# Performance work log

Hardware: AMD Instinct MI355X
Metric: run time of the kernel (lower is better)

## Reference

```python
import jax, jax.numpy as jnp
import numpy as np

EMBED = 768
HEADS = 12
HEAD_DIM = EMBED // HEADS
STREAMS = 4
SK_ITERS = 20
MLP_HIDDEN = 3072
EPS_SK = 1e-8
EPS_LN = 1e-5


def setup_inputs() -> dict:
    key = jax.random.key(0)
    ks = jax.random.split(key, 16)
    w = lambda k, shape: (jax.random.normal(k, shape, dtype=jnp.float32) * 0.02)
    return {
        "x": jax.random.normal(ks[0], (8, 1024, EMBED), dtype=jnp.float32),
        "ln1_g": jnp.ones((EMBED,), jnp.float32),
        "ln1_b": jnp.zeros((EMBED,), jnp.float32),
        "ln2_g": jnp.ones((EMBED,), jnp.float32),
        "ln2_b": jnp.zeros((EMBED,), jnp.float32),
        "qkv_w": w(ks[1], (3 * EMBED, EMBED)),
        "qkv_b": jnp.zeros((3 * EMBED,), jnp.float32),
        "proj_w": w(ks[2], (EMBED, EMBED)),
        "proj_b": jnp.zeros((EMBED,), jnp.float32),
        "fc1_w": w(ks[3], (MLP_HIDDEN, EMBED)),
        "fc1_b": jnp.zeros((MLP_HIDDEN,), jnp.float32),
        "fc2_w": w(ks[4], (EMBED, MLP_HIDDEN)),
        "fc2_b": jnp.zeros((EMBED,), jnp.float32),
        "a_hres": w(ks[5], (STREAMS, STREAMS)),
        "a_hpre": w(ks[6], (STREAMS,)),
        "a_hpost": w(ks[7], (STREAMS,)),
        "m_hres": w(ks[8], (STREAMS, STREAMS)),
        "m_hpre": w(ks[9], (STREAMS,)),
        "m_hpost": w(ks[10], (STREAMS,)),
    }


def layernorm(x, g, b):
    mu = x.mean(-1, keepdims=True)
    var = ((x - mu) ** 2).mean(-1, keepdims=True)
    return (x - mu) * jax.lax.rsqrt(var + EPS_LN) * g + b


def sinkhorn_knopp(logits):
    # logits: (n, n) -> doubly-stochastic (n, n); batch expansion in torch is redundant
    A = jnp.exp(logits)
    for _ in range(SK_ITERS):
        A = A / (A.sum(-1, keepdims=True) + EPS_SK)
        A = A / (A.sum(-2, keepdims=True) + EPS_SK)
    return A


def attention(x, qkv_w, qkv_b, proj_w, proj_b):
    B, N, D = x.shape
    qkv = x @ qkv_w.T + qkv_b                      # (B, N, 3D)
    qkv = qkv.reshape(B, N, 3, HEADS, HEAD_DIM)
    q, k, v = jnp.moveaxis(qkv, 2, 0)              # each (B, N, H, hd)
    scale = HEAD_DIM ** -0.5
    scores = jnp.einsum('bqhd,bkhd->bhqk', q, k) * scale
    attn = jax.nn.softmax(scores, axis=-1)
    out = jnp.einsum('bhqk,bkhd->bqhd', attn, v).reshape(B, N, D)
    return out @ proj_w.T + proj_b


def mlp(x, fc1_w, fc1_b, fc2_w, fc2_b):
    h = jax.nn.gelu(x @ fc1_w.T + fc1_b, approximate=False)
    return h @ fc2_w.T + fc2_b


def mhc(x, hres_logits, hpre_logits, hpost_logits, transform_fn):
    B, L, D = x.shape
    n, c = STREAMS, D // STREAMS
    xs = x.reshape(B, L, n, c)
    H_res = sinkhorn_knopp(hres_logits)            # (n, n)
    H_pre = jax.nn.softmax(hpre_logits)            # (n,)
    H_post = jax.nn.softmax(hpost_logits)          # (n,)
    x_pre = jnp.einsum('n,blnc->blc', H_pre, xs)   # weighted sum over streams
    x_pre_full = jnp.tile(x_pre, (1, 1, n))        # (B, L, D)
    t = transform_fn(x_pre_full)
    t_mean = t.reshape(B, L, n, c).mean(axis=2)    # (B, L, c)
    out = (jnp.einsum('nm,blmc->blnc', H_res, xs)
           + H_post[None, None, :, None] * t_mean[:, :, None, :])
    return out.reshape(B, L, D)


def reference(x, ln1_g, ln1_b, ln2_g, ln2_b, qkv_w, qkv_b, proj_w, proj_b,
              fc1_w, fc1_b, fc2_w, fc2_b,
              a_hres, a_hpre, a_hpost, m_hres, m_hpre, m_hpost):
    x = mhc(x, a_hres, a_hpre, a_hpost,
            lambda h: attention(layernorm(h, ln1_g, ln1_b), qkv_w, qkv_b, proj_w, proj_b))
    x = mhc(x, m_hres, m_hpre, m_hpost,
            lambda h: mlp(layernorm(h, ln2_g, ln2_b), fc1_w, fc1_b, fc2_w, fc2_b))
    return x
```

## Files before the change

kernel.cpp:

```cpp
#include <hip/hip_runtime.h>
#include <hip/hip_bf16.h>
#include <cstdint>
#include <cstddef>

#define EMBED 768
#define STREAMS 4
#define CHUNK 192
#define HEADS 12
#define HD 64
#define SEQ 1024
#define BATCH 8
#define TOKENS (BATCH * SEQ)
#define MLPH 3072

typedef __bf16 bf16;
typedef __bf16 bf16x4 __attribute__((ext_vector_type(4)));
typedef __bf16 bf16x8 __attribute__((ext_vector_type(8)));
typedef float f32x4 __attribute__((ext_vector_type(4)));
typedef float f32x16 __attribute__((ext_vector_type(16)));

#define GLDS16(gp, lp)                                                        \
  __builtin_amdgcn_global_load_lds(                                           \
      (const __attribute__((address_space(1))) void*)(gp),                    \
      (__attribute__((address_space(3))) void*)(lp), 16, 0, 0)

#define BARRIER() do { asm volatile("" ::: "memory");                         \
  __builtin_amdgcn_s_barrier(); asm volatile("" ::: "memory"); } while (0)

#define CVT_NQ 442368
#define CVT_NP 147456
#define CVT_N1 589824
#define CVT_TOT (CVT_NQ + CVT_NP + 2 * CVT_N1)
__global__ __launch_bounds__(256) void head_kernel(
    const float* __restrict__ x, const float* __restrict__ ln1_g,
    const float* __restrict__ ln1_b, bf16* __restrict__ LN,
    const float* __restrict__ qw, const float* __restrict__ pw,
    const float* __restrict__ f1w, const float* __restrict__ f2w,
    bf16* __restrict__ Wq, bf16* __restrict__ Wp,
    bf16* __restrict__ W1, bf16* __restrict__ W2,
    const float* ar, const float* ap, const float* ao,
    const float* mr, const float* mp, const float* mo, float* HS) {
  const int tid = threadIdx.x;
  if (blockIdx.x < 2048) {
    int i = blockIdx.x * 256 + tid;
    const int st = 2048 * 256;
    for (; i < CVT_TOT; i += st) {
      const float* src; bf16* dst; int off;
      if (i < CVT_NQ)                      { src = qw;  dst = Wq; off = i; }
      else if (i < CVT_NQ + CVT_NP)        { src = pw;  dst = Wp; off = i - CVT_NQ; }
      else if (i < CVT_NQ + CVT_NP + CVT_N1){ src = f1w; dst = W1; off = i - CVT_NQ - CVT_NP; }
      else                                 { src = f2w; dst = W2; off = i - CVT_NQ - CVT_NP - CVT_N1; }
      const float4 v = ((const float4*)src)[off];
      bf16x4 o = {(bf16)v.x, (bf16)v.y, (bf16)v.z, (bf16)v.w};
      *(bf16x4*)(dst + (size_t)off * 4) = o;
    }
    return;
  }
  if (blockIdx.x == 4096) {
    if (tid != 0) return;
    const float* L[2] = {ar, mr};
    const float* P[2] = {ap, mp};
    const float* O[2] = {ao, mo};
    for (int s = 0; s < 2; ++s) {
      float A[16];
      for (int i = 0; i < 16; ++i) A[i] = expf(L[s][i]);
      for (int it = 0; it < 20; ++it) {
        for (int r = 0; r < 4; ++r) {
          float rs = A[4*r] + A[4*r+1] + A[4*r+2] + A[4*r+3] + 1e-8f;
          for (int c = 0; c < 4; ++c) A[4*r+c] /= rs;
        }
        for (int c = 0; c < 4; ++c) {
          float cs = A[c] + A[4+c] + A[8+c] + A[12+c] + 1e-8f;
          for (int r = 0; r < 4; ++r) A[4*r+c] /= cs;
        }
      }
      float* dst = HS + s * 24;
      for (int i = 0; i < 16; ++i) dst[i] = A[i];
      {
        float m = fmaxf(fmaxf(P[s][0], P[s][1]), fmaxf(P[s][2], P[s][3]));
        float e[4], t = 0.f;
        for (int i = 0; i < 4; ++i) { e[i] = expf(P[s][i] - m); t += e[i]; }
        for (int i = 0; i < 4; ++i) dst[16 + i] = e[i] / t;
      }
      {
        float m = fmaxf(fmaxf(O[s][0], O[s][1]), fmaxf(O[s][2], O[s][3]));
        float e[4], t = 0.f;
        for (int i = 0; i < 4; ++i) { e[i] = expf(O[s][i] - m); t += e[i]; }
        for (int i = 0; i < 4; ++i) dst[20 + i] = e[i] / t;
      }
    }
    return;
  }
  const int t = (blockIdx.x - 2048) * 4 + (tid >> 6);
  const int l = tid & 63;
  float H0, H1, H2, H3;
  {
    const float p0 = ap[0], p1 = ap[1], p2 = ap[2], p3 = ap[3];
    const float m = fmaxf(fmaxf(p0, p1), fmaxf(p2, p3));
    const float e0 = __expf(p0 - m), e1 = __expf(p1 - m),
                e2 = __expf(p2 - m), e3 = __expf(p3 - m);
    const float inv = 1.f / (e0 + e1 + e2 + e3);
    H0 = e0 * inv; H1 = e1 * inv; H2 = e2 * inv; H3 = e3 * inv;
  }
  const float* xr = x + (size_t)t * EMBED;
  float sv[3];
  #pragma unroll
  for (int k = 0; k < 3; ++k) {
    const int c = l + 64 * k;
    sv[k] = H0*xr[c] + H1*xr[CHUNK+c] + H2*xr[2*CHUNK+c] + H3*xr[3*CHUNK+c];
  }
  float sum = sv[0] + sv[1] + sv[2];
  float sq  = sv[0]*sv[0] + sv[1]*sv[1] + sv[2]*sv[2];
  #pragma unroll
  for (int m = 1; m < 64; m <<= 1) {
    sum += __shfl_xor(sum, m);
    sq  += __shfl_xor(sq, m);
  }
  const float mu = sum * (1.f / CHUNK);
  const float rs = rsqrtf(sq * (1.f / CHUNK) - mu * mu + 1e-5f);
  bf16* orow = LN + (size_t)t * EMBED;
  #pragma unroll
  for (int k = 0; k < 3; ++k) {
    const int c = l + 64 * k;
    const float sn = (sv[k] - mu) * rs;
    #pragma unroll
    for (int n = 0; n < 4; ++n) {
      const int d = n * CHUNK + c;
      orow[d] = (bf16)(sn * ln1_g[d] + ln1_b[d]);
    }
  }
}

template <int GELU, int KSPLIT>
__global__ __launch_bounds__(256, 2) void gemm_bt(
    const bf16* __restrict__ A, const bf16* __restrict__ B,
    const float* __restrict__ bias, bf16* __restrict__ C0,
    bf16* __restrict__ C1, int M, int N, int K) {
  constexpr int BM = 128, BN = 128, BK = 32;
  __shared__ bf16 sA[3][BM * BK];
  __shared__ bf16 sB[3][BN * BK];
  const int tid  = threadIdx.x;
  const int lane = tid & 63;
  const int Lw = blockIdx.y * gridDim.x + blockIdx.x;
  const int bandRows = gridDim.y >> 3;
  const int j = Lw >> 3;
  const int colIdx = j / bandRows;
  const int rowLoc = j - colIdx * bandRows;
  const int bm = ((Lw & 7) * bandRows + rowLoc) * BM;
  const int bn = colIdx * BN;
  const int wave = tid >> 6;
  const int wr = (wave >> 1) * 64;
  const int wc = (wave & 1) * 64;
  f32x16 acc[2][2] = {};
  const int tr = tid >> 2;
  const int gt = tid & 3;
  const int gsw = (gt ^ ((tr >> 1) & 3)) * 8;
  const int kbeg = (KSPLIT > 1) ? blockIdx.z * (K / KSPLIT) : 0;
  const bf16* Ag = A + (size_t)(bm + tr) * K + kbeg + gsw;
  const bf16* Bg = B + (size_t)(bn + tr) * K + kbeg + gsw;
  const int lofs = tr * BK + gt * 8;
  const int r31 = lane & 31, rh = lane >> 5;
  const int asw = (r31 >> 1) & 3;
  const int nst = K / KSPLIT / BK;
#define STAGE(buf, t)                                                         \
  do { const int bk_ = (t) * BK;                                              \
    GLDS16(Ag + bk_, sA[buf] + lofs);                                         \
    GLDS16(Ag + (size_t)64 * K + bk_, sA[buf] + lofs + 64 * BK);              \
    GLDS16(Bg + bk_, sB[buf] + lofs);                                         \
    GLDS16(Bg + (size_t)64 * K + bk_, sB[buf] + lofs + 64 * BK);              \
  } while (0)
  STAGE(0, 0);
  STAGE(1, 1);
  int cur = 0;
  for (int t = 0; t < nst; ++t) {
    if (t + 2 < nst) {
      const int nb = cur + 2 >= 3 ? cur - 1 : cur + 2;
      STAGE(nb, t + 2);
      asm volatile("s_waitcnt vmcnt(8)" ::: "memory");
    } else if (t + 1 < nst) {
      asm volatile("s_waitcnt vmcnt(4)" ::: "memory");
    } else {
      asm volatile("s_waitcnt vmcnt(0)" ::: "memory");
    }
    BARRIER();
    bf16x8 af[2][2], bfr[2][2];
    #pragma unroll
    for (int ks = 0; ks < 2; ++ks) {
      const int pos = ((ks * 2 + rh) ^ asw) * 8;
      #pragma unroll
      for (int i = 0; i < 2; ++i) {
        af[i][ks]  = *(const bf16x8*)(sA[cur] + (wr + i * 32 + r31) * BK + pos);
        bfr[i][ks] = *(const bf16x8*)(sB[cur] + (wc + i * 32 + r31) * BK + pos);
      }
    }
    #pragma unroll
    for (int ks = 0; ks < 2; ++ks)
      #pragma unroll
      for (int i = 0; i < 2; ++i)
        #pragma unroll
        for (int j2 = 0; j2 < 2; ++j2)
          acc[i][j2] = __builtin_amdgcn_mfma_f32_32x32x16_bf16(af[i][ks], bfr[j2][ks], acc[i][j2], 0, 0, 0);
    BARRIER();
    cur = cur == 2 ? 0 : cur + 1;
  }
#undef STAGE
  const bool second = (KSPLIT > 1) && (blockIdx.z != 0);
  bf16* Co = second ? C1 : C0;
  #pragma unroll
  for (int j2 = 0; j2 < 2; ++j2) {
    const int col = bn + wc + j2 * 32 + r31;
    const float bv = second ? 0.f : bias[col];
    #pragma unroll
    for (int i = 0; i < 2; ++i) {
      const int row0 = bm + wr + i * 32 + 4 * rh;
      #pragma unroll
      for (int reg = 0; reg < 16; ++reg) {
        const int row = row0 + (reg & 3) + 8 * (reg >> 2);
        float v = acc[i][j2][reg] + bv;
        if (GELU) {
          float u = 0.7978845608f * (v + 0.044715f * v * v * v);
          u = fmaxf(fminf(u, 15.f), -15.f);
          const float e = __expf(-2.f * u);
          v = v / (1.f + e);
        }
        Co[(size_t)row * N + col] = (bf16)v;
      }
    }
  }
}

__global__ __launch_bounds__(256) void vt_kernel(const bf16* __restrict__ qkv,
                                                 bf16* __restrict__ VT) {
  const int tt = blockIdx.x;
  const int bh = blockIdx.y;
  const int bb = bh / HEADS;
  const int h = bh - bb * HEADS;
  __shared__ bf16 sT[64 * 64];
  const int t = threadIdx.x;
  const int srow = t >> 3;
  const int g = t & 7;
  const int gs = ((g ^ (srow & 7)) * 8);
  const bf16* Vg = qkv + ((size_t)(bb * SEQ + tt * 64 + srow)) * 2304 + 1536 + h * 64;
  GLDS16(Vg + gs, sT + srow * 64 + g * 8);
  GLDS16(Vg + (size_t)32 * 2304 + gs, sT + (32 + srow) * 64 + g * 8);
  __syncthreads();
  const int hd = t >> 2;
  const int tg = (t & 3) * 16;
  bf16 tmp[16];
  #pragma unroll
  for (int j = 0; j < 16; ++j) {
    const int tok = tg + j;
    tmp[j] = sT[tok * 64 + (hd ^ ((tok & 7) << 3))];
  }
  bf16* op = VT + (size_t)bh * (HD * SEQ) + (size_t)hd * SEQ + tt * 64 + tg;
  *(bf16x8*)(op) = *(const bf16x8*)(tmp);
  *(bf16x8*)(op + 8) = *(const bf16x8*)(tmp + 8);
}

__global__ __launch_bounds__(512) void attn_kernel(
    const bf16* __restrict__ qkv, const bf16* __restrict__ VT,
    bf16* __restrict__ out) {
  const int lin = blockIdx.x;
  const int qt = (lin >> 3) & 7;
  const int bh = (lin & 7) + 8 * (lin >> 6);
  const int bb = bh / HEADS;
  const int h = bh - bb * HEADS;
  const int tid = threadIdx.x;
  const int lane = tid & 63;
  const int wave = tid >> 6;
  const size_t tokBase = (size_t)bb * SEQ;
  const int q0 = qt * 128;

  __shared__ bf16 sQ[128 * 64];
  __shared__ bf16 sK[2][64 * 64];
  __shared__ bf16 sV[2][80 * 64];

  for (int idx = tid; idx < 16 * 64; idx += 512) {
    const bf16 v = (idx < 64) ? (bf16)1.f : (bf16)0.f;
    sV[0][64 * 64 + idx] = v;
    sV[1][64 * 64 + idx] = v;
  }

  {
    #pragma unroll
    for (int kq = 0; kq < 2; ++kq) {
      const int slot = tid + kq * 512;
      const int qr = slot >> 3;
      const int qg = slot & 7;
      const bf16* Qg = qkv + (tokBase + q0 + qr) * 2304 + h * 64;
      GLDS16(Qg + ((qg ^ (qr & 7)) * 8), sQ + qr * 64 + qg * 8);
    }
  }
  const int srow = tid >> 3;
  const int g = tid & 7;
  const int gs = ((g ^ (srow & 7)) * 8);
  const bf16* Kbase = qkv + tokBase * 2304 + 768 + h * 64;
  const bf16* Vbase = VT + (size_t)bh * (HD * SEQ);
  GLDS16(Kbase + (size_t)srow * 2304 + gs, sK[0] + srow * 64 + g * 8);
  GLDS16(Vbase + (size_t)srow * SEQ + gs, sV[0] + srow * 64 + g * 8);
  __syncthreads();

  const int l15 = lane & 15, hi = lane >> 4;
  const int ksw = (l15 & 7) << 3;
  bf16x8 qf[2];
  {
    const int qrow = wave * 16 + l15;
    const int qsw = (qrow & 7) << 3;
    #pragma unroll
    for (int ks = 0; ks < 2; ++ks)
      qf[ks] = *(const bf16x8*)(sQ + qrow * 64 + ((hi * 8 + ks * 32) ^ qsw));
  }
  asm volatile("s_waitcnt lgkmcnt(0)" ::: "memory");

  f32x4 o[5] = {};

  for (int it = 0; it < SEQ / 64; ++it) {
    const int cur = it & 1;
    if (it + 1 < SEQ / 64) {
      const int kb = (it + 1) * 64;
      GLDS16(Kbase + (size_t)(kb + srow) * 2304 + gs, sK[cur ^ 1] + srow * 64 + g * 8);
      GLDS16(Vbase + (size_t)srow * SEQ + kb + gs, sV[cur ^ 1] + srow * 64 + g * 8);
      asm volatile("s_waitcnt vmcnt(2)" ::: "memory");
    } else {
      asm volatile("s_waitcnt vmcnt(0)" ::: "memory");
    }
    BARRIER();
    f32x4 s[4];
    __builtin_amdgcn_s_setprio(1);
    #pragma unroll
    for (int nj = 0; nj < 4; ++nj) {
      s[nj] = (f32x4){0.f, 0.f, 0.f, 0.f};
      #pragma unroll
      for (int ks = 0; ks < 2; ++ks) {
        bf16x8 kf = *(const bf16x8*)(sK[cur] + (nj * 16 + l15) * 64 + ((hi * 8 + ks * 32) ^ ksw));
        s[nj] = __builtin_amdgcn_mfma_f32_16x16x32_bf16(qf[ks], kf, s[nj], 0, 0, 0);
      }
    }
    __builtin_amdgcn_s_setprio(0);
    bf16* Pw = sQ + wave * (16 * 64);
    #pragma unroll
    for (int r = 0; r < 4; ++r) {
      const int prow = hi * 4 + r;
      const int psw = (prow & 7) << 3;
      #pragma unroll
      for (int nj = 0; nj < 4; ++nj)
        Pw[prow * 64 + ((nj * 16 + l15) ^ psw)] = (bf16)__expf(s[nj][r] * 0.125f);
    }
    __builtin_amdgcn_s_setprio(1);
    #pragma unroll
    for (int ks = 0; ks < 2; ++ks) {
      bf16x8 pa = *(const bf16x8*)(Pw + l15 * 64 + ((hi * 8 + ks * 32) ^ ksw));
      #pragma unroll
      for (int nj = 0; nj < 5; ++nj) {
        bf16x8 vb = *(const bf16x8*)(sV[cur] + (nj * 16 + l15) * 64 + ((hi * 8 + ks * 32) ^ ksw));
        o[nj] = __builtin_amdgcn_mfma_f32_16x16x32_bf16(pa, vb, o[nj], 0, 0, 0);
      }
    }
    __builtin_amdgcn_s_setprio(0);
    BARRIER();
  }
  #pragma unroll
  for (int r = 0; r < 4; ++r) {
    const float lsum = __shfl(o[4][r], hi << 4, 64);
    const float inv = 1.f / lsum;
    const size_t row = tokBase + q0 + wave * 16 + hi * 4 + r;
    bf16* orow = out + row * EMBED + h * 64;
    #pragma unroll
    for (int nj = 0; nj < 4; ++nj)
      orow[nj * 16 + l15] = (bf16)(o[nj][r] * inv);
  }
}

template <int TWO>
__global__ __launch_bounds__(256) void combine_preln_kernel(
    const float* __restrict__ x, const bf16* __restrict__ t,
    const bf16* __restrict__ t2,
    const float* __restrict__ Hres, const float* __restrict__ Hpost,
    const float* __restrict__ Hpre2,
    const float* __restrict__ g2, const float* __restrict__ b2,
    bf16* __restrict__ X2, bf16* __restrict__ LN) {
  const int tok = blockIdx.x * 4 + (threadIdx.x >> 6);
  const int l = threadIdx.x & 63;
  const float* xr = x + (size_t)tok * EMBED;
  const bf16* tr = t + (size_t)tok * EMBED;
  const bf16* t2r = t2 + (size_t)tok * EMBED;
  bf16* orow = X2 + (size_t)tok * EMBED;
  const float Hr0 = Hres[0], Hr1 = Hres[1], Hr2 = Hres[2], Hr3 = Hres[3];
  const float Hr4 = Hres[4], Hr5 = Hres[5], Hr6 = Hres[6], Hr7 = Hres[7];
  const float Hr8 = Hres[8], Hr9 = Hres[9], HrA = Hres[10], HrB = Hres[11];
  const float HrC = Hres[12], HrD = Hres[13], HrE = Hres[14], HrF = Hres[15];
  const float Hp0 = Hpost[0], Hp1 = Hpost[1], Hp2 = Hpost[2], Hp3 = Hpost[3];
  const float He0 = Hpre2[0], He1 = Hpre2[1], He2 = Hpre2[2], He3 = Hpre2[3];
  float sv[3];
  #pragma unroll
  for (int k = 0; k < 3; ++k) {
    const int c = l + 64 * k;
    const float x0 = xr[c], x1 = xr[CHUNK + c], x2v = xr[2 * CHUNK + c], x3 = xr[3 * CHUNK + c];
    float tm = (float)tr[c] + (float)tr[CHUNK + c] + (float)tr[2 * CHUNK + c] + (float)tr[3 * CHUNK + c];
    if (TWO)
      tm += (float)t2r[c] + (float)t2r[CHUNK + c] + (float)t2r[2 * CHUNK + c] + (float)t2r[3 * CHUNK + c];
    tm *= 0.25f;
    const float v0 = Hr0*x0 + Hr1*x1 + Hr2*x2v + Hr3*x3 + Hp0 * tm;
    const float v1 = Hr4*x0 + Hr5*x1 + Hr6*x2v + Hr7*x3 + Hp1 * tm;
    const float v2 = Hr8*x0 + Hr9*x1 + HrA*x2v + HrB*x3 + Hp2 * tm;
    const float v3 = HrC*x0 + HrD*x1 + HrE*x2v + HrF*x3 + Hp3 * tm;
    orow[c] = (bf16)v0;
    orow[CHUNK + c] = (bf16)v1;
    orow[2 * CHUNK + c] = (bf16)v2;
    orow[3 * CHUNK + c] = (bf16)v3;
    sv[k] = He0 * v0 + He1 * v1 + He2 * v2 + He3 * v3;
  }
  float sum = sv[0] + sv[1] + sv[2];
  float sq  = sv[0]*sv[0] + sv[1]*sv[1] + sv[2]*sv[2];
  #pragma unroll
  for (int m = 1; m < 64; m <<= 1) {
    sum += __shfl_xor(sum, m);
    sq  += __shfl_xor(sq, m);
  }
  const float mu = sum * (1.f / CHUNK);
  const float rs = rsqrtf(sq * (1.f / CHUNK) - mu * mu + 1e-5f);
  bf16* lrow = LN + (size_t)tok * EMBED;
  #pragma unroll
  for (int k = 0; k < 3; ++k) {
    const int c = l + 64 * k;
    const float sn = (sv[k] - mu) * rs;
    #pragma unroll
    for (int n = 0; n < 4; ++n) {
      const int d = n * CHUNK + c;
      lrow[d] = (bf16)(sn * g2[d] + b2[d]);
    }
  }
}

template <int TWO>
__global__ void combine_kernel(const bf16* __restrict__ xs, const bf16* __restrict__ t,
                               const bf16* __restrict__ t2,
                               const float* __restrict__ Hres, const float* __restrict__ Hpost,
                               float* __restrict__ outp) {
  const int idx = blockIdx.x * 256 + threadIdx.x;
  if (idx >= TOKENS * CHUNK) return;
  const int tok = idx / CHUNK;
  const int c = idx - tok * CHUNK;
  const bf16* xr = xs + (size_t)tok * EMBED + c;
  const bf16* tr = t + (size_t)tok * EMBED + c;
  const float x0 = (float)xr[0], x1 = (float)xr[CHUNK],
              x2 = (float)xr[2 * CHUNK], x3 = (float)xr[3 * CHUNK];
  float tm = (float)tr[0] + (float)tr[CHUNK] + (float)tr[2 * CHUNK] + (float)tr[3 * CHUNK];
  if (TWO) {
    const bf16* t2r = t2 + (size_t)tok * EMBED + c;
    tm += (float)t2r[0] + (float)t2r[CHUNK] + (float)t2r[2 * CHUNK] + (float)t2r[3 * CHUNK];
  }
  tm *= 0.25f;
  #pragma unroll
  for (int n = 0; n < 4; ++n) {
    const float v = Hres[4*n+0]*x0 + Hres[4*n+1]*x1 + Hres[4*n+2]*x2 + Hres[4*n+3]*x3
                  + Hpost[n] * tm;
    outp[(size_t)tok * EMBED + n * CHUNK + c] = v;
  }
}

extern "C" void kernel_launch(void* const* d_in, const int* in_sizes, int n_in,
                              void* d_out, int out_size, void* d_ws, size_t ws_size,
                              hipStream_t stream) {
  const float* x       = (const float*)d_in[0];
  const float* ln1_g   = (const float*)d_in[1];
  const float* ln1_b   = (const float*)d_in[2];
  const float* ln2_g   = (const float*)d_in[3];
  const float* ln2_b   = (const float*)d_in[4];
  const float* qkv_w   = (const float*)d_in[5];
  const float* qkv_b   = (const float*)d_in[6];
  const float* proj_w  = (const float*)d_in[7];
  const float* proj_b  = (const float*)d_in[8];
  const float* fc1_w   = (const float*)d_in[9];
  const float* fc1_b   = (const float*)d_in[10];
  const float* fc2_w   = (const float*)d_in[11];
  const float* fc2_b   = (const float*)d_in[12];
  const float* a_hres  = (const float*)d_in[13];
  const float* a_hpre  = (const float*)d_in[14];
  const float* a_hpost = (const float*)d_in[15];
  const float* m_hres  = (const float*)d_in[16];
  const float* m_hpre  = (const float*)d_in[17];
  const float* m_hpost = (const float*)d_in[18];

  char* ws = (char*)d_ws;
  float* HS = (float*)(ws);
  bf16* Wq  = (bf16*)(ws + 1024);
  bf16* Wp  = (bf16*)(ws + 1024 + 3538944);
  bf16* W1  = (bf16*)(ws + 1024 + 3538944 + 1179648);
  bf16* W2  = (bf16*)(ws + 1024 + 3538944 + 1179648 + 4718592);
  bf16* LN  = (bf16*)(ws + 14156800);
  bf16* T   = (bf16*)(ws + 26739712);
  bf16* PT  = (bf16*)(ws + 39322624);
  bf16* X2  = (bf16*)(ws + 51905536);
  bf16* QKV = (bf16*)(ws + 77071360);
  bf16* AO  = (bf16*)(ws + 114820096);
  bf16* Hm  = (bf16*)(ws + 77071360);
  bf16* VT  = LN;

  head_kernel<<<4097, 256, 0, stream>>>(
      x, ln1_g, ln1_b, LN,
      qkv_w, proj_w, fc1_w, fc2_w, Wq, Wp, W1, W2,
      a_hres, a_hpre, a_hpost, m_hres, m_hpre, m_hpost, HS);

  gemm_bt<0, 1><<<dim3(2304 / 128, TOKENS / 128), 256, 0, stream>>>(
      LN, Wq, qkv_b, QKV, nullptr, TOKENS, 2304, 768);
  vt_kernel<<<dim3(16, 96), 256, 0, stream>>>(QKV, VT);
  attn_kernel<<<768, 512, 0, stream>>>(QKV, VT, AO);
  gemm_bt<0, 2><<<dim3(768 / 128, TOKENS / 128, 2), 256, 0, stream>>>(
      AO, Wp, proj_b, T, PT, TOKENS, 768, 768);
  combine_preln_kernel<1><<<TOKENS / 4, 256, 0, stream>>>(
      x, T, PT, HS + 0, HS + 20, HS + 24 + 16, ln2_g, ln2_b, X2, LN);

  gemm_bt<1, 1><<<dim3(3072 / 128, TOKENS / 128), 256, 0, stream>>>(
      LN, W1, fc1_b, Hm, nullptr, TOKENS, 3072, 768);
  gemm_bt<0, 2><<<dim3(768 / 128, TOKENS / 128, 2), 256, 0, stream>>>(
      Hm, W2, fc2_b, T, PT, TOKENS, 768, 3072);
  combine_kernel<1><<<(TOKENS * CHUNK + 255) / 256, 256, 0, stream>>>(
      X2, T, PT, HS + 24, HS + 24 + 20, (float*)d_out);
}
```

Measured before the change: 305.5 us.

## Switch attention kernel to 32x32x16 MFMA with 4 waves of 32 query rows

Reworks the attention kernel from 8 waves each handling 16 query rows with 16x16x32 MFMAs to 4 waves each handling 32 rows with 32x32x16 MFMAs. The row-sum trick moves to a separate ones buffer and a third accumulator. K/V staging now issues two loads per thread per buffer. The aim is to cut LDS fragment reads per FLOP and get higher MFMA throughput, at the cost of fewer waves per block and more accumulator registers.

```diff
diff --git a/kernel.cpp b/kernel.cpp
--- a/kernel.cpp
+++ b/kernel.cpp
@@ -257,7 +257,7 @@
   *(bf16x8*)(op + 8) = *(const bf16x8*)(tmp + 8);
 }
 
-__global__ __launch_bounds__(512) void attn_kernel(
+__global__ __launch_bounds__(256) void attn_kernel(
     const bf16* __restrict__ qkv, const bf16* __restrict__ VT,
     bf16* __restrict__ out) {
   const int lin = blockIdx.x;
@@ -273,101 +273,113 @@
 
   __shared__ bf16 sQ[128 * 64];
   __shared__ bf16 sK[2][64 * 64];
-  __shared__ bf16 sV[2][80 * 64];
-
-  for (int idx = tid; idx < 16 * 64; idx += 512) {
-    const bf16 v = (idx < 64) ? (bf16)1.f : (bf16)0.f;
-    sV[0][64 * 64 + idx] = v;
-    sV[1][64 * 64 + idx] = v;
-  }
-
-  {
-    #pragma unroll
-    for (int kq = 0; kq < 2; ++kq) {
-      const int slot = tid + kq * 512;
-      const int qr = slot >> 3;
-      const int qg = slot & 7;
-      const bf16* Qg = qkv + (tokBase + q0 + qr) * 2304 + h * 64;
-      GLDS16(Qg + ((qg ^ (qr & 7)) * 8), sQ + qr * 64 + qg * 8);
-    }
-  }
-  const int srow = tid >> 3;
+  __shared__ bf16 sV[2][64 * 64];
+  __shared__ bf16 sOnes[32 * 64];
+
+  for (int idx = tid; idx < 32 * 64; idx += 256)
+    sOnes[idx] = (idx < 64) ? (bf16)1.f : (bf16)0.f;
+
+  #pragma unroll
+  for (int kq = 0; kq < 4; ++kq) {
+    const int slot = tid + kq * 256;
+    const int qr = slot >> 3;
+    const int qg = slot & 7;
+    const bf16* Qg = qkv + (tokBase + q0 + qr) * 2304 + h * 64;
+    GLDS16(Qg + ((qg ^ (qr & 7)) * 8), sQ + qr * 64 + qg * 8);
+  }
+  const int sr0 = tid >> 3;
   const int g = tid & 7;
-  const int gs = ((g ^ (srow & 7)) * 8);
   const bf16* Kbase = qkv + tokBase * 2304 + 768 + h * 64;
   const bf16* Vbase = VT + (size_t)bh * (HD * SEQ);
-  GLDS16(Kbase + (size_t)srow * 2304 + gs, sK[0] + srow * 64 + g * 8);
-  GLDS16(Vbase + (size_t)srow * SEQ + gs, sV[0] + srow * 64 + g * 8);
+#define STAGEKV(buf, kb)                                                      \
+  do {                                                                        \
+    _Pragma("unroll")                                                         \
+    for (int hf = 0; hf < 2; ++hf) {                                          \
+      const int row = sr0 + hf * 32;                                          \
+      const int gsw = (g ^ (row & 7)) * 8;                                    \
+      GLDS16(Kbase + (size_t)((kb) + row) * 2304 + gsw,                       \
+             sK[buf] + row * 64 + g * 8);                                     \
+      GLDS16(Vbase + (size_t)row * SEQ + (kb) + gsw,                          \
+             sV[buf] + row * 64 + g * 8);                                     \
+    }                                                                         \
+  } while (0)
+  STAGEKV(0, 0);
   __syncthreads();
 
-  const int l15 = lane & 15, hi = lane >> 4;
-  const int ksw = (l15 & 7) << 3;
-  bf16x8 qf[2];
+  const int r31 = lane & 31, rh = lane >> 5;
+  bf16x8 qf[4];
   {
-    const int qrow = wave * 16 + l15;
+    const int qrow = wave * 32 + r31;
     const int qsw = (qrow & 7) << 3;
     #pragma unroll
-    for (int ks = 0; ks < 2; ++ks)
-      qf[ks] = *(const bf16x8*)(sQ + qrow * 64 + ((hi * 8 + ks * 32) ^ qsw));
+    for (int ks = 0; ks < 4; ++ks)
+      qf[ks] = *(const bf16x8*)(sQ + qrow * 64 + ((ks * 16 + rh * 8) ^ qsw));
   }
   asm volatile("s_waitcnt lgkmcnt(0)" ::: "memory");
 
-  f32x4 o[5] = {};
+  f32x16 o[2] = {};
+  f32x16 o2 = {};
+  const int psw31 = (r31 & 7) << 3;
 
   for (int it = 0; it < SEQ / 64; ++it) {
     const int cur = it & 1;
     if (it + 1 < SEQ / 64) {
-      const int kb = (it + 1) * 64;
-      GLDS16(Kbase + (size_t)(kb + srow) * 2304 + gs, sK[cur ^ 1] + srow * 64 + g * 8);
-      GLDS16(Vbase + (size_t)srow * SEQ + kb + gs, sV[cur ^ 1] + srow * 64 + g * 8);
-      asm volatile("s_waitcnt vmcnt(2)" ::: "memory");
+      STAGEKV(cur ^ 1, (it + 1) * 64);
+      asm volatile("s_waitcnt vmcnt(4)" ::: "memory");
     } else {
       asm volatile("s_waitcnt vmcnt(0)" ::: "memory");
     }
     BARRIER();
-    f32x4 s[4];
+    f32x16 s[2] = {};
     __builtin_amdgcn_s_setprio(1);
     #pragma unroll
-    for (int nj = 0; nj < 4; ++nj) {
-      s[nj] = (f32x4){0.f, 0.f, 0.f, 0.f};
+    for (int ks = 0; ks < 4; ++ks) {
+      const int pos = ks * 16 + rh * 8;
       #pragma unroll
-      for (int ks = 0; ks < 2; ++ks) {
-        bf16x8 kf = *(const bf16x8*)(sK[cur] + (nj * 16 + l15) * 64 + ((hi * 8 + ks * 32) ^ ksw));
-        s[nj] = __builtin_amdgcn_mfma_f32_16x16x32_bf16(qf[ks], kf, s[nj], 0, 0, 0);
+      for (int j = 0; j < 2; ++j) {
+        const int krow = j * 32 + r31;
+        bf16x8 kf = *(const bf16x8*)(sK[cur] + krow * 64 + (pos ^ ((krow & 7) << 3)));
+        s[j] = __builtin_amdgcn_mfma_f32_32x32x16_bf16(qf[ks], kf, s[j], 0, 0, 0);
       }
     }
     __builtin_amdgcn_s_setprio(0);
-    bf16* Pw = sQ + wave * (16 * 64);
-    #pragma unroll
-    for (int r = 0; r < 4; ++r) {
-      const int prow = hi * 4 + r;
-      const int psw = (prow & 7) << 3;
+    bf16* Pw = sQ + wave * (32 * 64);
+    #pragma unroll
+    for (int j = 0; j < 2; ++j)
       #pragma unroll
-      for (int nj = 0; nj < 4; ++nj)
-        Pw[prow * 64 + ((nj * 16 + l15) ^ psw)] = (bf16)__expf(s[nj][r] * 0.125f);
-    }
+      for (int r = 0; r < 16; ++r) {
+        const int prow = (r & 3) + 8 * (r >> 2) + 4 * rh;
+        const int col = j * 32 + r31;
+        Pw[prow * 64 + (col ^ ((prow & 7) << 3))] = (bf16)__expf(s[j][r] * 0.125f);
+      }
     __builtin_amdgcn_s_setprio(1);
     #pragma unroll
-    for (int ks = 0; ks < 2; ++ks) {
-      bf16x8 pa = *(const bf16x8*)(Pw + l15 * 64 + ((hi * 8 + ks * 32) ^ ksw));
+    for (int ks = 0; ks < 4; ++ks) {
+      const int pos = ks * 16 + rh * 8;
+      bf16x8 pa = *(const bf16x8*)(Pw + r31 * 64 + (pos ^ psw31));
       #pragma unroll
-      for (int nj = 0; nj < 5; ++nj) {
-        bf16x8 vb = *(const bf16x8*)(sV[cur] + (nj * 16 + l15) * 64 + ((hi * 8 + ks * 32) ^ ksw));
-        o[nj] = __builtin_amdgcn_mfma_f32_16x16x32_bf16(pa, vb, o[nj], 0, 0, 0);
-      }
+      for (int j2 = 0; j2 < 2; ++j2) {
+        const int vrow = j2 * 32 + r31;
+        bf16x8 vb = *(const bf16x8*)(sV[cur] + vrow * 64 + (pos ^ ((vrow & 7) << 3)));
+        o[j2] = __builtin_amdgcn_mfma_f32_32x32x16_bf16(pa, vb, o[j2], 0, 0, 0);
+      }
+      bf16x8 ob = *(const bf16x8*)(sOnes + r31 * 64 + pos);
+      o2 = __builtin_amdgcn_mfma_f32_32x32x16_bf16(pa, ob, o2, 0, 0, 0);
     }
     __builtin_amdgcn_s_setprio(0);
     BARRIER();
   }
-  #pragma unroll
-  for (int r = 0; r < 4; ++r) {
-    const float lsum = __shfl(o[4][r], hi << 4, 64);
+#undef STAGEKV
+  #pragma unroll
+  for (int r = 0; r < 16; ++r) {
+    const int q = (r & 3) + 8 * (r >> 2) + 4 * rh;
+    const float lsum = __shfl(o2[r], rh << 5, 64);
     const float inv = 1.f / lsum;
-    const size_t row = tokBase + q0 + wave * 16 + hi * 4 + r;
+    const size_t row = tokBase + q0 + wave * 32 + q;
     bf16* orow = out + row * EMBED + h * 64;
     #pragma unroll
-    for (int nj = 0; nj < 4; ++nj)
-      orow[nj * 16 + l15] = (bf16)(o[nj][r] * inv);
+    for (int j2 = 0; j2 < 2; ++j2)
+      orow[j2 * 32 + r31] = (bf16)(o[j2][r] * inv);
   }
 }
 
@@ -505,7 +517,7 @@
   gemm_bt<0, 1><<<dim3(2304 / 128, TOKENS / 128), 256, 0, stream>>>(
       LN, Wq, qkv_b, QKV, nullptr, TOKENS, 2304, 768);
   vt_kernel<<<dim3(16, 96), 256, 0, stream>>>(QKV, VT);
-  attn_kernel<<<768, 512, 0, stream>>>(QKV, VT, AO);
+  attn_kernel<<<768, 256, 0, stream>>>(QKV, VT, AO);
   gemm_bt<0, 2><<<dim3(768 / 128, TOKENS / 128, 2), 256, 0, stream>>>(
       AO, Wp, proj_b, T, PT, TOKENS, 768, 768);
   combine_preln_kernel<1><<<TOKENS / 4, 256, 0, stream>>>(
```

After: 323.7 us. +5.9%, slower.
